# Kernel optimization log

Measured on AMD Instinct MI355X. Metric: run time of the kernel, lower is better.

The kernel has to match this reference:

```python
import jax, jax.numpy as jnp
import numpy as np

# bitsandbytes FP4 code table (magnitudes), signed -> 16 codes (two zeros, harmless)
_FP4_MAGS = np.array([0.0, 0.0052083333, 1.0/6.0, 0.25, 1.0/3.0, 0.5, 2.0/3.0, 1.0], dtype=np.float32)
_FP4_CODES = np.sort(np.concatenate([-_FP4_MAGS, _FP4_MAGS])).astype(np.float32)
_FP4_BOUNDS = ((_FP4_CODES[:-1] + _FP4_CODES[1:]) * 0.5).astype(np.float32)
_BLOCK = 64  # bnb default FP4 blocksize


def fp4_roundtrip(w):
    """Simulate bnb quantize_fp4 -> dequantize_fp4 (blockwise absmax + nearest FP4 code)."""
    shp = w.shape
    wf = w.reshape(-1, _BLOCK)                              # [n_blocks, 64]
    absmax = jnp.max(jnp.abs(wf), axis=1, keepdims=True)    # per-block scale
    n = wf / jnp.maximum(absmax, 1e-12)                     # normalized to [-1, 1]
    idx = jnp.searchsorted(jnp.asarray(_FP4_BOUNDS), n)     # nearest-code index
    deq = jnp.asarray(_FP4_CODES)[idx] * absmax             # dequantized values
    return deq.reshape(shp)


def setup_inputs() -> dict:
    key = jax.random.key(0)
    k1, k2 = jax.random.split(key)
    in_features, out_features, tokens = 4096, 11008, 8192
    x = jax.random.normal(k1, (tokens, in_features), dtype=jnp.float32)
    weight = jax.random.normal(k2, (out_features, in_features), dtype=jnp.float32) * 0.1
    bias = jnp.zeros((out_features,), dtype=jnp.float32)
    return {"x": x, "weight": weight, "bias": bias}


def reference(x, weight, bias):
    # forward path with quantized weights: dequantize FP4 then matmul + bias
    w = fp4_roundtrip(weight)                # [out, in]
    return jnp.matmul(x, w.T) + bias         # [tokens, out]
```

## Files before the change

kernel.cpp:

```cpp
#include <hip/hip_runtime.h>
#include <hip/hip_bf16.h>
#include <stdint.h>

#define M_DIM 8192
#define N_DIM 11008
#define K_DIM 4096

typedef __attribute__((ext_vector_type(8))) short bf16x8;
typedef __attribute__((ext_vector_type(4))) float f32x4;

__device__ const float kCodes[16] = {
    -1.0f, -(float)(2.0 / 3.0), -0.5f, -(float)(1.0 / 3.0), -0.25f,
    -(float)(1.0 / 6.0), -0.0052083333f, -0.0f,
    0.0f, 0.0052083333f, (float)(1.0 / 6.0), 0.25f,
    (float)(1.0 / 3.0), 0.5f, (float)(2.0 / 3.0), 1.0f};

__device__ __forceinline__ float fp4_bound(int i) {
  return (kCodes[i] + kCodes[i + 1]) * 0.5f;
}

__device__ __forceinline__ unsigned short f2bf(float f) {
  uint32_t u = __float_as_uint(f);
  u = (u + 0x7FFFu + ((u >> 16) & 1u)) >> 16;
  return (unsigned short)u;
}

__device__ __forceinline__ float fp4_rt(float w, float d, float am) {
  float n = w / d;
  int idx = 0;
#pragma unroll
  for (int i = 0; i < 15; ++i) idx += (n > fp4_bound(i)) ? 1 : 0;
  return kCodes[idx] * am;
}

__global__ void quant_fp4_kernel(const float* __restrict__ W,
                                 unsigned short* __restrict__ Wq) {
  int t = blockIdx.x * 256 + threadIdx.x;
  size_t base = (size_t)t * 4;
  float4 v = *reinterpret_cast<const float4*>(W + base);
  float am = fmaxf(fmaxf(fabsf(v.x), fabsf(v.y)), fmaxf(fabsf(v.z), fabsf(v.w)));
  am = fmaxf(am, __shfl_xor(am, 1));
  am = fmaxf(am, __shfl_xor(am, 2));
  am = fmaxf(am, __shfl_xor(am, 4));
  am = fmaxf(am, __shfl_xor(am, 8));
  float d = fmaxf(am, 1e-12f);
  ushort4 o;
  o.x = f2bf(fp4_rt(v.x, d, am));
  o.y = f2bf(fp4_rt(v.y, d, am));
  o.z = f2bf(fp4_rt(v.z, d, am));
  o.w = f2bf(fp4_rt(v.w, d, am));
  *reinterpret_cast<ushort4*>(Wq + base) = o;
}

__device__ __forceinline__ uint32_t pack2(float lo, float hi) {
  return (uint32_t)f2bf(lo) | ((uint32_t)f2bf(hi) << 16);
}

__global__ void cast_bf16_kernel(const float* __restrict__ X,
                                 uint32_t* __restrict__ Y) {
  int t = blockIdx.x * 256 + threadIdx.x;
  size_t base = (size_t)t * 8;
  float4 a = *reinterpret_cast<const float4*>(X + base);
  float4 b = *reinterpret_cast<const float4*>(X + base + 4);
  uint4 o;
  o.x = pack2(a.x, a.y);
  o.y = pack2(a.z, a.w);
  o.z = pack2(b.x, b.y);
  o.w = pack2(b.z, b.w);
  *reinterpret_cast<uint4*>(Y + (size_t)t * 4) = o;
}

#define GLOAD(src, dst)                                                        \
  __builtin_amdgcn_global_load_lds(                                           \
      (const __attribute__((address_space(1))) void*)(src),                   \
      (__attribute__((address_space(3))) void*)(dst), 16, 0, 0)

#define PHASE_MID()                                                            \
  __builtin_amdgcn_s_barrier();                                                \
  asm volatile("s_waitcnt lgkmcnt(0)" ::: "memory");                           \
  __builtin_amdgcn_sched_barrier(0);                                           \
  __builtin_amdgcn_s_setprio(1);

#define PHASE_END()                                                            \
  __builtin_amdgcn_s_setprio(0);                                               \
  __builtin_amdgcn_sched_barrier(0);                                           \
  __builtin_amdgcn_s_barrier();

#define PHASE_END_VM()                                                         \
  __builtin_amdgcn_s_setprio(0);                                               \
  __builtin_amdgcn_sched_barrier(0);                                           \
  asm volatile("s_waitcnt vmcnt(4)" ::: "memory");                             \
  __builtin_amdgcn_s_barrier();

__global__ __launch_bounds__(512, 2) void gemm256_kernel(
    const short* __restrict__ A, const short* __restrict__ B,
    const float* __restrict__ bias, float* __restrict__ C) {
  __shared__ short lds[2][4][8192];

  const int tid = threadIdx.x;
  const int wave = tid >> 6;
  const int lane = tid & 63;
  const int l15 = lane & 15;
  const int q4 = lane >> 4;
  const int wm = wave >> 2;
  const int wn = wave & 3;

  const int bid = blockIdx.x;
  const int g = bid & 7;
  const int idx = bid >> 3;
  const int brow = (g * 4 + (idx & 3)) * 256;
  const int bcol = (idx >> 2) * 256;

  const int srow = tid >> 3;
  const int scol = ((tid & 7) ^ ((tid >> 3) & 7)) << 3;
  const short* Asrc = A + (size_t)(brow + srow) * K_DIM + scol;
  const short* Bsrc = B + (size_t)(bcol + srow) * K_DIM + scol;
  const int wu0 = wave * 512;
  const int wu1 = 4096 + wave * 512;

  auto stageA = [&](int buf, int half, int t) {
    const short* s = Asrc + (size_t)half * 128 * K_DIM + t * 64;
    GLOAD(s, &lds[buf][half][wu0]);
    GLOAD(s + (size_t)64 * K_DIM, &lds[buf][half][wu1]);
  };
  auto stageB = [&](int buf, int half, int t) {
    const short* s = Bsrc + (size_t)half * 128 * K_DIM + t * 64;
    GLOAD(s, &lds[buf][2 + half][wu0]);
    GLOAD(s + (size_t)64 * K_DIM, &lds[buf][2 + half][wu1]);
  };

  const int offk0 = ((q4 ^ (l15 & 7)) << 4);
  const int offk1 = offk0 ^ 64;
  const char* aP[2] = {(const char*)&lds[0][wm][0] + l15 * 128,
                       (const char*)&lds[1][wm][0] + l15 * 128};
  const char* bP[2] = {
      (const char*)&lds[0][2 + (wn >> 1)][0] + (wn & 1) * 8192 + l15 * 128,
      (const char*)&lds[1][2 + (wn >> 1)][0] + (wn & 1) * 8192 + l15 * 128};

  f32x4 acc[8][4] = {};

  stageB(0, 0, 0);
  stageB(0, 1, 0);
  stageA(0, 0, 0);
  stageA(0, 1, 0);
  stageB(1, 0, 1);
  stageB(1, 1, 1);
  asm volatile("s_waitcnt vmcnt(4)" ::: "memory");
  __builtin_amdgcn_s_barrier();

  for (int i = 0; i < 32; ++i) {
    const int t1 = 2 * i + 1;
    const int t2 = (2 * i + 2 < 64) ? 2 * i + 2 : 63;
    const int t3 = (2 * i + 3 < 64) ? 2 * i + 3 : 63;

    bf16x8 af[4], bf[2][4];

#pragma unroll
    for (int m = 0; m < 4; ++m)
      af[m] = *(const bf16x8*)(aP[0] + m * 2048 + offk0);
#pragma unroll
    for (int n = 0; n < 4; ++n)
      bf[0][n] = *(const bf16x8*)(bP[0] + n * 2048 + offk0);
#pragma unroll
    for (int n = 0; n < 4; ++n)
      bf[1][n] = *(const bf16x8*)(bP[0] + n * 2048 + offk1);
    stageA(1, 0, t1);
    PHASE_MID();
#pragma unroll
    for (int m = 0; m < 4; ++m)
#pragma unroll
      for (int n = 0; n < 4; ++n)
        acc[m][n] = __builtin_amdgcn_mfma_f32_16x16x32_bf16(af[m], bf[0][n],
                                                            acc[m][n], 0, 0, 0);
    PHASE_END();

#pragma unroll
    for (int m = 0; m < 4; ++m)
      af[m] = *(const bf16x8*)(aP[0] + (4 + m) * 2048 + offk0);
    stageA(1, 1, t1);
    PHASE_MID();
#pragma unroll
    for (int m = 0; m < 4; ++m)
#pragma unroll
      for (int n = 0; n < 4; ++n)
        acc[4 + m][n] = __builtin_amdgcn_mfma_f32_16x16x32_bf16(
            af[m], bf[0][n], acc[4 + m][n], 0, 0, 0);
    PHASE_END();

#pragma unroll
    for (int m = 0; m < 4; ++m)
      af[m] = *(const bf16x8*)(aP[0] + m * 2048 + offk1);
    stageB(0, 0, t2);
    PHASE_MID();
#pragma unroll
    for (int m = 0; m < 4; ++m)
#pragma unroll
      for (int n = 0; n < 4; ++n)
        acc[m][n] = __builtin_amdgcn_mfma_f32_16x16x32_bf16(af[m], bf[1][n],
                                                            acc[m][n], 0, 0, 0);
    PHASE_END();

#pragma unroll
    for (int m = 0; m < 4; ++m)
      af[m] = *(const bf16x8*)(aP[0] + (4 + m) * 2048 + offk1);
    stageB(0, 1, t2);
    PHASE_MID();
#pragma unroll
    for (int m = 0; m < 4; ++m)
#pragma unroll
      for (int n = 0; n < 4; ++n)
        acc[4 + m][n] = __builtin_amdgcn_mfma_f32_16x16x32_bf16(
            af[m], bf[1][n], acc[4 + m][n], 0, 0, 0);
    PHASE_END_VM();

#pragma unroll
    for (int m = 0; m < 4; ++m)
      af[m] = *(const bf16x8*)(aP[1] + m * 2048 + offk0);
#pragma unroll
    for (int n = 0; n < 4; ++n)
      bf[0][n] = *(const bf16x8*)(bP[1] + n * 2048 + offk0);
#pragma unroll
    for (int n = 0; n < 4; ++n)
      bf[1][n] = *(const bf16x8*)(bP[1] + n * 2048 + offk1);
    stageA(0, 0, t2);
    PHASE_MID();
#pragma unroll
    for (int m = 0; m < 4; ++m)
#pragma unroll
      for (int n = 0; n < 4; ++n)
        acc[m][n] = __builtin_amdgcn_mfma_f32_16x16x32_bf16(af[m], bf[0][n],
                                                            acc[m][n], 0, 0, 0);
    PHASE_END();

#pragma unroll
    for (int m = 0; m < 4; ++m)
      af[m] = *(const bf16x8*)(aP[1] + (4 + m) * 2048 + offk0);
    stageA(0, 1, t2);
    PHASE_MID();
#pragma unroll
    for (int m = 0; m < 4; ++m)
#pragma unroll
      for (int n = 0; n < 4; ++n)
        acc[4 + m][n] = __builtin_amdgcn_mfma_f32_16x16x32_bf16(
            af[m], bf[0][n], acc[4 + m][n], 0, 0, 0);
    PHASE_END();

#pragma unroll
    for (int m = 0; m < 4; ++m)
      af[m] = *(const bf16x8*)(aP[1] + m * 2048 + offk1);
    stageB(1, 0, t3);
    PHASE_MID();
#pragma unroll
    for (int m = 0; m < 4; ++m)
#pragma unroll
      for (int n = 0; n < 4; ++n)
        acc[m][n] = __builtin_amdgcn_mfma_f32_16x16x32_bf16(af[m], bf[1][n],
                                                            acc[m][n], 0, 0, 0);
    PHASE_END();

#pragma unroll
    for (int m = 0; m < 4; ++m)
      af[m] = *(const bf16x8*)(aP[1] + (4 + m) * 2048 + offk1);
    stageB(1, 1, t3);
    PHASE_MID();
#pragma unroll
    for (int m = 0; m < 4; ++m)
#pragma unroll
      for (int n = 0; n < 4; ++n)
        acc[4 + m][n] = __builtin_amdgcn_mfma_f32_16x16x32_bf16(
            af[m], bf[1][n], acc[4 + m][n], 0, 0, 0);
    PHASE_END_VM();
  }

  const int crow0 = brow + wm * 128 + q4 * 4;
  const int ccol0 = bcol + wn * 64 + l15;
#pragma unroll
  for (int n = 0; n < 4; ++n) {
    const float bv = bias[ccol0 + n * 16];
#pragma unroll
    for (int m = 0; m < 8; ++m) {
      const size_t rb = (size_t)(crow0 + m * 16) * N_DIM + (ccol0 + n * 16);
#pragma unroll
      for (int j = 0; j < 4; ++j) C[rb + (size_t)j * N_DIM] = acc[m][n][j] + bv;
    }
  }
}

extern "C" void kernel_launch(void* const* d_in, const int* in_sizes, int n_in,
                              void* d_out, int out_size, void* d_ws, size_t ws_size,
                              hipStream_t stream) {
  const float* x = (const float*)d_in[0];
  const float* w = (const float*)d_in[1];
  const float* bias = (const float*)d_in[2];
  float* out = (float*)d_out;

  unsigned short* wq = (unsigned short*)d_ws;
  unsigned short* xb = wq + (size_t)N_DIM * K_DIM;

  {
    int nt = N_DIM * K_DIM / 4;
    quant_fp4_kernel<<<nt / 256, 256, 0, stream>>>(w, wq);
  }
  {
    int nt = M_DIM * K_DIM / 8;
    cast_bf16_kernel<<<nt / 256, 256, 0, stream>>>(x, (uint32_t*)xb);
  }
  {
    gemm256_kernel<<<dim3(1376), 512, 0, stream>>>((const short*)xb,
                                                   (const short*)wq, bias, out);
  }
}
```

Baseline: 751.7 us.

## Software-pipeline LDS fragment loads across MFMA phases with partial lgkmcnt waits

Restructures the main GEMM loop so LDS fragment reads for the next phase are issued before the current phase's MFMAs. Each phase waits only on lgkmcnt(4/8) instead of draining all LDS traffic, and drops the mid-phase barrier. Fragments are double-buffered in registers (afA/afB, bfA/bfB), and global-to-LDS staging is regrouped with full vmcnt(0) drains at buffer switches. The aim is to hide LDS latency behind matrix math and cut barrier count. The costs are more register pressure and a risk of ordering hazards if the lgkmcnt counts or barrier placement are wrong.

Measured after the change: 750.5 us. About the same (-0.1%).

```diff
diff --git a/kernel.cpp b/kernel.cpp
--- a/kernel.cpp
+++ b/kernel.cpp
@@ -75,21 +75,25 @@
       (const __attribute__((address_space(1))) void*)(src),                   \
       (__attribute__((address_space(3))) void*)(dst), 16, 0, 0)
 
-#define PHASE_MID()                                                            \
-  __builtin_amdgcn_s_barrier();                                                \
-  asm volatile("s_waitcnt lgkmcnt(0)" ::: "memory");                           \
+#define WAIT_LGKM4()                                                           \
+  asm volatile("s_waitcnt lgkmcnt(4)" ::: "memory");                           \
   __builtin_amdgcn_sched_barrier(0);                                           \
   __builtin_amdgcn_s_setprio(1);
 
-#define PHASE_END()                                                            \
+#define WAIT_LGKM8()                                                           \
+  asm volatile("s_waitcnt lgkmcnt(8)" ::: "memory");                           \
+  __builtin_amdgcn_sched_barrier(0);                                           \
+  __builtin_amdgcn_s_setprio(1);
+
+#define ENDBAR()                                                               \
   __builtin_amdgcn_s_setprio(0);                                               \
   __builtin_amdgcn_sched_barrier(0);                                           \
   __builtin_amdgcn_s_barrier();
 
-#define PHASE_END_VM()                                                         \
+#define ENDBAR_VM0()                                                           \
   __builtin_amdgcn_s_setprio(0);                                               \
   __builtin_amdgcn_sched_barrier(0);                                           \
-  asm volatile("s_waitcnt vmcnt(4)" ::: "memory");                             \
+  asm volatile("s_waitcnt vmcnt(0)" ::: "memory");                             \
   __builtin_amdgcn_s_barrier();
 
 __global__ __launch_bounds__(512, 2) void gemm256_kernel(
@@ -138,138 +142,140 @@
       (const char*)&lds[1][2 + (wn >> 1)][0] + (wn & 1) * 8192 + l15 * 128};
 
   f32x4 acc[8][4] = {};
+  bf16x8 afA[4], afB[4], bfA[4], bfB[4];
 
   stageB(0, 0, 0);
   stageB(0, 1, 0);
   stageA(0, 0, 0);
   stageA(0, 1, 0);
   stageB(1, 0, 1);
-  stageB(1, 1, 1);
-  asm volatile("s_waitcnt vmcnt(4)" ::: "memory");
+  asm volatile("s_waitcnt vmcnt(2)" ::: "memory");
   __builtin_amdgcn_s_barrier();
+#pragma unroll
+  for (int m = 0; m < 4; ++m) afA[m] = *(const bf16x8*)(aP[0] + m * 2048 + offk0);
+#pragma unroll
+  for (int n = 0; n < 4; ++n) bfA[n] = *(const bf16x8*)(bP[0] + n * 2048 + offk0);
 
   for (int i = 0; i < 32; ++i) {
     const int t1 = 2 * i + 1;
     const int t2 = (2 * i + 2 < 64) ? 2 * i + 2 : 63;
     const int t3 = (2 * i + 3 < 64) ? 2 * i + 3 : 63;
 
-    bf16x8 af[4], bf[2][4];
-
-#pragma unroll
-    for (int m = 0; m < 4; ++m)
-      af[m] = *(const bf16x8*)(aP[0] + m * 2048 + offk0);
+#pragma unroll
+    for (int m = 0; m < 4; ++m)
+      afB[m] = *(const bf16x8*)(aP[0] + (4 + m) * 2048 + offk0);
+    stageB(1, 1, t1);
+    WAIT_LGKM4();
+#pragma unroll
+    for (int m = 0; m < 4; ++m)
+#pragma unroll
+      for (int n = 0; n < 4; ++n)
+        acc[m][n] = __builtin_amdgcn_mfma_f32_16x16x32_bf16(afA[m], bfA[n],
+                                                            acc[m][n], 0, 0, 0);
+    ENDBAR();
+
+#pragma unroll
+    for (int m = 0; m < 4; ++m)
+      afA[m] = *(const bf16x8*)(aP[0] + m * 2048 + offk1);
 #pragma unroll
     for (int n = 0; n < 4; ++n)
-      bf[0][n] = *(const bf16x8*)(bP[0] + n * 2048 + offk0);
+      bfB[n] = *(const bf16x8*)(bP[0] + n * 2048 + offk1);
+    stageA(1, 0, t1);
+    stageA(1, 1, t1);
+    WAIT_LGKM8();
+#pragma unroll
+    for (int m = 0; m < 4; ++m)
+#pragma unroll
+      for (int n = 0; n < 4; ++n)
+        acc[4 + m][n] = __builtin_amdgcn_mfma_f32_16x16x32_bf16(
+            afB[m], bfA[n], acc[4 + m][n], 0, 0, 0);
+    ENDBAR();
+
+#pragma unroll
+    for (int m = 0; m < 4; ++m)
+      afB[m] = *(const bf16x8*)(aP[0] + (4 + m) * 2048 + offk1);
+    WAIT_LGKM4();
+#pragma unroll
+    for (int m = 0; m < 4; ++m)
+#pragma unroll
+      for (int n = 0; n < 4; ++n)
+        acc[m][n] = __builtin_amdgcn_mfma_f32_16x16x32_bf16(afA[m], bfB[n],
+                                                            acc[m][n], 0, 0, 0);
+    ENDBAR_VM0();
+
+#pragma unroll
+    for (int m = 0; m < 4; ++m)
+      afA[m] = *(const bf16x8*)(aP[1] + m * 2048 + offk0);
 #pragma unroll
     for (int n = 0; n < 4; ++n)
-      bf[1][n] = *(const bf16x8*)(bP[0] + n * 2048 + offk1);
-    stageA(1, 0, t1);
-    PHASE_MID();
-#pragma unroll
-    for (int m = 0; m < 4; ++m)
-#pragma unroll
-      for (int n = 0; n < 4; ++n)
-        acc[m][n] = __builtin_amdgcn_mfma_f32_16x16x32_bf16(af[m], bf[0][n],
+      bfA[n] = *(const bf16x8*)(bP[1] + n * 2048 + offk0);
+    stageB(0, 0, t2);
+    WAIT_LGKM8();
+#pragma unroll
+    for (int m = 0; m < 4; ++m)
+#pragma unroll
+      for (int n = 0; n < 4; ++n)
+        acc[4 + m][n] = __builtin_amdgcn_mfma_f32_16x16x32_bf16(
+            afB[m], bfB[n], acc[4 + m][n], 0, 0, 0);
+    ENDBAR();
+
+#pragma unroll
+    for (int m = 0; m < 4; ++m)
+      afB[m] = *(const bf16x8*)(aP[1] + (4 + m) * 2048 + offk0);
+    stageB(0, 1, t2);
+    WAIT_LGKM4();
+#pragma unroll
+    for (int m = 0; m < 4; ++m)
+#pragma unroll
+      for (int n = 0; n < 4; ++n)
+        acc[m][n] = __builtin_amdgcn_mfma_f32_16x16x32_bf16(afA[m], bfA[n],
                                                             acc[m][n], 0, 0, 0);
-    PHASE_END();
-
-#pragma unroll
-    for (int m = 0; m < 4; ++m)
-      af[m] = *(const bf16x8*)(aP[0] + (4 + m) * 2048 + offk0);
-    stageA(1, 1, t1);
-    PHASE_MID();
+    ENDBAR();
+
+#pragma unroll
+    for (int m = 0; m < 4; ++m)
+      afA[m] = *(const bf16x8*)(aP[1] + m * 2048 + offk1);
+#pragma unroll
+    for (int n = 0; n < 4; ++n)
+      bfB[n] = *(const bf16x8*)(bP[1] + n * 2048 + offk1);
+    stageA(0, 0, t2);
+    stageA(0, 1, t2);
+    WAIT_LGKM8();
 #pragma unroll
     for (int m = 0; m < 4; ++m)
 #pragma unroll
       for (int n = 0; n < 4; ++n)
         acc[4 + m][n] = __builtin_amdgcn_mfma_f32_16x16x32_bf16(
-            af[m], bf[0][n], acc[4 + m][n], 0, 0, 0);
-    PHASE_END();
-
-#pragma unroll
-    for (int m = 0; m < 4; ++m)
-      af[m] = *(const bf16x8*)(aP[0] + m * 2048 + offk1);
-    stageB(0, 0, t2);
-    PHASE_MID();
-#pragma unroll
-    for (int m = 0; m < 4; ++m)
-#pragma unroll
-      for (int n = 0; n < 4; ++n)
-        acc[m][n] = __builtin_amdgcn_mfma_f32_16x16x32_bf16(af[m], bf[1][n],
+            afB[m], bfA[n], acc[4 + m][n], 0, 0, 0);
+    ENDBAR();
+
+#pragma unroll
+    for (int m = 0; m < 4; ++m)
+      afB[m] = *(const bf16x8*)(aP[1] + (4 + m) * 2048 + offk1);
+    WAIT_LGKM4();
+#pragma unroll
+    for (int m = 0; m < 4; ++m)
+#pragma unroll
+      for (int n = 0; n < 4; ++n)
+        acc[m][n] = __builtin_amdgcn_mfma_f32_16x16x32_bf16(afA[m], bfB[n],
                                                             acc[m][n], 0, 0, 0);
-    PHASE_END();
-
-#pragma unroll
-    for (int m = 0; m < 4; ++m)
-      af[m] = *(const bf16x8*)(aP[0] + (4 + m) * 2048 + offk1);
-    stageB(0, 1, t2);
-    PHASE_MID();
+    ENDBAR_VM0();
+
+#pragma unroll
+    for (int m = 0; m < 4; ++m)
+      afA[m] = *(const bf16x8*)(aP[0] + m * 2048 + offk0);
+#pragma unroll
+    for (int n = 0; n < 4; ++n)
+      bfA[n] = *(const bf16x8*)(bP[0] + n * 2048 + offk0);
+    stageB(1, 0, t3);
+    WAIT_LGKM8();
 #pragma unroll
     for (int m = 0; m < 4; ++m)
 #pragma unroll
       for (int n = 0; n < 4; ++n)
         acc[4 + m][n] = __builtin_amdgcn_mfma_f32_16x16x32_bf16(
-            af[m], bf[1][n], acc[4 + m][n], 0, 0, 0);
-    PHASE_END_VM();
-
-#pragma unroll
-    for (int m = 0; m < 4; ++m)
-      af[m] = *(const bf16x8*)(aP[1] + m * 2048 + offk0);
-#pragma unroll
-    for (int n = 0; n < 4; ++n)
-      bf[0][n] = *(const bf16x8*)(bP[1] + n * 2048 + offk0);
-#pragma unroll
-    for (int n = 0; n < 4; ++n)
-      bf[1][n] = *(const bf16x8*)(bP[1] + n * 2048 + offk1);
-    stageA(0, 0, t2);
-    PHASE_MID();
-#pragma unroll
-    for (int m = 0; m < 4; ++m)
-#pragma unroll
-      for (int n = 0; n < 4; ++n)
-        acc[m][n] = __builtin_amdgcn_mfma_f32_16x16x32_bf16(af[m], bf[0][n],
-                                                            acc[m][n], 0, 0, 0);
-    PHASE_END();
-
-#pragma unroll
-    for (int m = 0; m < 4; ++m)
-      af[m] = *(const bf16x8*)(aP[1] + (4 + m) * 2048 + offk0);
-    stageA(0, 1, t2);
-    PHASE_MID();
-#pragma unroll
-    for (int m = 0; m < 4; ++m)
-#pragma unroll
-      for (int n = 0; n < 4; ++n)
-        acc[4 + m][n] = __builtin_amdgcn_mfma_f32_16x16x32_bf16(
-            af[m], bf[0][n], acc[4 + m][n], 0, 0, 0);
-    PHASE_END();
-
-#pragma unroll
-    for (int m = 0; m < 4; ++m)
-      af[m] = *(const bf16x8*)(aP[1] + m * 2048 + offk1);
-    stageB(1, 0, t3);
-    PHASE_MID();
-#pragma unroll
-    for (int m = 0; m < 4; ++m)
-#pragma unroll
-      for (int n = 0; n < 4; ++n)
-        acc[m][n] = __builtin_amdgcn_mfma_f32_16x16x32_bf16(af[m], bf[1][n],
-                                                            acc[m][n], 0, 0, 0);
-    PHASE_END();
-
-#pragma unroll
-    for (int m = 0; m < 4; ++m)
-      af[m] = *(const bf16x8*)(aP[1] + (4 + m) * 2048 + offk1);
-    stageB(1, 1, t3);
-    PHASE_MID();
-#pragma unroll
-    for (int m = 0; m < 4; ++m)
-#pragma unroll
-      for (int n = 0; n < 4; ++n)
-        acc[4 + m][n] = __builtin_amdgcn_mfma_f32_16x16x32_bf16(
-            af[m], bf[1][n], acc[4 + m][n], 0, 0, 0);
-    PHASE_END_VM();
+            afB[m], bfB[n], acc[4 + m][n], 0, 0, 0);
+    ENDBAR();
   }
 
   const int crow0 = brow + wm * 128 + q4 * 4;
```
